# Kernel tuning notes

Hardware: AMD Instinct MI355X
Metric: run time of the kernel (lower is better)

The kernel has to match this reference:

```python
import jax, jax.numpy as jnp
import numpy as np

BN_EPS = 1e-5
L2_EPS = 1e-12


def _gconv(x, adj, W, b):
    # x: [B, N, F_in], adj: [N, N] (densified sparse), W: [F_in, F_out]
    y = jnp.einsum('rc,bcf->brf', adj, x)          # sparse aggregation (spmm)
    y = jnp.einsum('brf,fo->bro', y, W) + b        # dense transform + bias
    n = jnp.sqrt(jnp.sum(y * y, axis=2, keepdims=True))
    return y / jnp.maximum(n, L2_EPS)              # F.normalize(p=2, dim=2)


def _bn3(x):
    # BatchNorm1d over channel dim=1 (roinum), batch stats, affine = identity
    m = jnp.mean(x, axis=(0, 2), keepdims=True)
    v = jnp.var(x, axis=(0, 2), keepdims=True)
    return (x - m) / jnp.sqrt(v + BN_EPS)


def _bn2(x):
    m = jnp.mean(x, axis=0, keepdims=True)
    v = jnp.var(x, axis=0, keepdims=True)
    return (x - m) / jnp.sqrt(v + BN_EPS)


def setup_inputs() -> dict:
    key = jax.random.key(0)
    ks = jax.random.split(key, 20)
    B, N, F_in, H, E, L = 256, 400, 400, 64, 64, 2
    NNZ = 16000
    pred_in = H * 2 + E  # hidden*(num_layers-1) + embedding = 192
    nhid = H

    def xavier(k, fi, fo):
        s = np.sqrt(6.0 / (fi + fo))
        return jax.random.uniform(k, (fi, fo), jnp.float32, -s, s)

    return {
        'x': jax.random.normal(ks[0], (B, N, F_in), jnp.float32),
        'adj_rows': jax.random.randint(ks[1], (NNZ,), 0, N, jnp.int32),
        'adj_cols': jax.random.randint(ks[2], (NNZ,), 0, N, jnp.int32),
        'adj_vals': jax.random.uniform(ks[3], (NNZ,), jnp.float32),
        'W1': xavier(ks[4], F_in, H), 'b1': jnp.zeros((H,), jnp.float32),
        'W2': xavier(ks[5], H, H),    'b2': jnp.zeros((H,), jnp.float32),
        'W3': xavier(ks[6], H, E),    'b3': jnp.zeros((E,), jnp.float32),
        'fc1_W': xavier(ks[7], pred_in, nhid), 'fc1_b': jnp.zeros((nhid,), jnp.float32),
        'fc2_W': xavier(ks[8], nhid, nhid),    'fc2_b': jnp.zeros((nhid,), jnp.float32),
        'fc3_W': xavier(ks[9], nhid, L),       'fc3_b': jnp.zeros((L,), jnp.float32),
    }


def reference(x, adj_rows, adj_cols, adj_vals,
              W1, b1, W2, b2, W3, b3,
              fc1_W, fc1_b, fc2_W, fc2_b, fc3_W, fc3_b):
    N = x.shape[1]
    adj = jnp.zeros((N, N), x.dtype).at[adj_rows, adj_cols].add(adj_vals)

    x1 = _bn3(jax.nn.relu(_gconv(x, adj, W1, b1)))
    out1 = jnp.max(x1, axis=1)                     # [B, H]
    x2 = _bn3(jax.nn.relu(_gconv(x1, adj, W2, b2)))
    out2 = jnp.max(x2, axis=1)                     # [B, H]
    x3 = _gconv(x2, adj, W3, b3)                   # [B, N, E]
    out3 = jnp.max(x3, axis=1)                     # [B, E]

    h = jnp.concatenate([out1, out2, out3], axis=1)  # [B, 2H+E]
    h = _bn2(jax.nn.relu(h @ fc1_W + fc1_b))
    h = _bn2(jax.nn.relu(h @ fc2_W + fc2_b))
    ypred = h @ fc3_W + fc3_b
    return ypred, x3
```

## Files before the change

### kernel.cpp

```cpp
#include <hip/hip_runtime.h>
#include <hip/hip_bf16.h>
#include <math.h>

#define Bb   256
#define Nn   400
#define FIN  400
#define Hh   64
#define NNZ  16000
#define Mrows (Bb*Nn)
#define KP   416
#define UTP  416
#define UPAD 420
#define BH_COUNT 16384.0f

typedef unsigned int  u32x2 __attribute__((ext_vector_type(2)));
typedef unsigned int  u32x4 __attribute__((ext_vector_type(4)));
typedef __bf16        bf16x8 __attribute__((ext_vector_type(8)));
typedef float         f32x4 __attribute__((ext_vector_type(4)));

__device__ __forceinline__ unsigned int f2bf(float x) {
    unsigned int u = __builtin_bit_cast(unsigned int, x);
    return (u + 0x7FFFu + ((u >> 16) & 1u)) >> 16;
}
__device__ __forceinline__ float bf2f(unsigned int h) {
    unsigned int u = h << 16;
    return __builtin_bit_cast(float, u);
}

__global__ void initk(float* __restrict__ Adf, float* __restrict__ stats,
                      unsigned short* __restrict__ Ut) {
    int t = blockIdx.x * blockDim.x + threadIdx.x;
    if (t < Nn * KP) Adf[t] = 0.f;
    if (t < 1600) stats[t] = 0.f;
    if (t < Bb * Hh * 16) {
        int bh = t >> 4, k = Nn + (t & 15);
        Ut[(size_t)bh * UTP + k] = 0;
    }
}

__global__ void scatAk(const int* __restrict__ rows, const int* __restrict__ cols,
                       const float* __restrict__ vals, float* __restrict__ Adf) {
    int i = blockIdx.x * blockDim.x + threadIdx.x;
    if (i < NNZ) atomicAdd(&Adf[rows[i] * KP + cols[i]], vals[i]);
}

__global__ void cvtAk(const float* __restrict__ Adf, unsigned short* __restrict__ Adbf) {
    int i = blockIdx.x * blockDim.x + threadIdx.x;
    if (i < Nn * KP) Adbf[i] = (unsigned short)f2bf(Adf[i]);
}

__global__ __launch_bounds__(256) void wprep(
        const float* __restrict__ W1, const float* __restrict__ W2,
        const float* __restrict__ W3,
        unsigned short* __restrict__ T1h, unsigned short* __restrict__ T1l,
        unsigned short* __restrict__ T2h, unsigned short* __restrict__ T2l,
        unsigned short* __restrict__ T3h, unsigned short* __restrict__ T3l) {
    const int w = blockIdx.x >> 6;
    const int c = blockIdx.x & 63;
    const float* W = (w == 0) ? W1 : (w == 1) ? W2 : W3;
    const int KT   = (w == 0) ? FIN : Hh;
    const int KPAD = (w == 0) ? 416 : 64;
    unsigned short* Th = (w == 0) ? T1h : (w == 1) ? T2h : T3h;
    unsigned short* Tl = (w == 0) ? T1l : (w == 1) ? T2l : T3l;

    for (int k = threadIdx.x; k < KPAD; k += 256) {
        float v = (k < KT) ? W[k * 64 + c] : 0.f;
        unsigned int hb = f2bf(v);
        Th[c * KPAD + k] = (unsigned short)hb;
        Tl[c * KPAD + k] = (unsigned short)f2bf(v - bf2f(hb));
    }
}

__global__ __launch_bounds__(256) void xg400(
        const float* __restrict__ A,
        const unsigned short* __restrict__ Wth,
        const unsigned short* __restrict__ Wtl,
        unsigned short* __restrict__ Ut) {
    const int tid  = threadIdx.x;
    const int wv   = tid >> 6;
    const int lane = tid & 63;
    const int cl   = lane & 15;
    const int g    = lane >> 4;
    const int m0   = blockIdx.x * 128;
    const int rowA = m0 + wv * 32 + cl;
    const int rowB = rowA + 16;

    f32x4 acc[2][4];
#pragma unroll
    for (int t2 = 0; t2 < 2; ++t2)
#pragma unroll
        for (int n = 0; n < 4; ++n) acc[t2][n] = f32x4{0.f, 0.f, 0.f, 0.f};

    auto loadA = [&](int s, float4& l0, float4& h0, float4& l1, float4& h1) {
        int kk = s * 32 + g * 8;
        int kc = kk > 392 ? 392 : kk;
        const float* p = &A[(size_t)rowA * FIN + kc];
        l0 = *reinterpret_cast<const float4*>(p);
        h0 = *reinterpret_cast<const float4*>(p + 4);
        const float* q = &A[(size_t)rowB * FIN + kc];
        l1 = *reinterpret_cast<const float4*>(q);
        h1 = *reinterpret_cast<const float4*>(q + 4);
    };
    auto loadW = [&](int s, u32x4* dst) {
        int kk = s * 32 + g * 8;
#pragma unroll
        for (int n = 0; n < 4; ++n) {
            dst[n]     = *reinterpret_cast<const u32x4*>(&Wth[(size_t)(n * 16 + cl) * 416 + kk]);
            dst[4 + n] = *reinterpret_cast<const u32x4*>(&Wtl[(size_t)(n * 16 + cl) * 416 + kk]);
        }
    };
    auto split = [&](const float4& lo, const float4& hi, bf16x8& ah, bf16x8& al) {
        float v0 = lo.x, v1 = lo.y, v2 = lo.z, v3 = lo.w;
        float v4 = hi.x, v5 = hi.y, v6 = hi.z, v7 = hi.w;
        unsigned h0, h1;
        u32x4 hw, lw;
        h0 = f2bf(v0); h1 = f2bf(v1);
        hw[0] = h0 | (h1 << 16);
        lw[0] = f2bf(v0 - bf2f(h0)) | (f2bf(v1 - bf2f(h1)) << 16);
        h0 = f2bf(v2); h1 = f2bf(v3);
        hw[1] = h0 | (h1 << 16);
        lw[1] = f2bf(v2 - bf2f(h0)) | (f2bf(v3 - bf2f(h1)) << 16);
        h0 = f2bf(v4); h1 = f2bf(v5);
        hw[2] = h0 | (h1 << 16);
        lw[2] = f2bf(v4 - bf2f(h0)) | (f2bf(v5 - bf2f(h1)) << 16);
        h0 = f2bf(v6); h1 = f2bf(v7);
        hw[3] = h0 | (h1 << 16);
        lw[3] = f2bf(v6 - bf2f(h0)) | (f2bf(v7 - bf2f(h1)) << 16);
        ah = __builtin_bit_cast(bf16x8, hw);
        al = __builtin_bit_cast(bf16x8, lw);
    };

    float4 cAl0, cAh0, cAl1, cAh1, nAl0, nAh0, nAl1, nAh1;
    u32x4  cW[8], nW[8];
    loadA(0, cAl0, cAh0, cAl1, cAh1);
    loadW(0, cW);

    for (int s = 0; s < 13; ++s) {
        if (s < 12) {
            loadA(s + 1, nAl0, nAh0, nAl1, nAh1);
            loadW(s + 1, nW);
        }
        bf16x8 ah0, al0, ah1, al1;
        split(cAl0, cAh0, ah0, al0);
        split(cAl1, cAh1, ah1, al1);
#pragma unroll
        for (int n = 0; n < 4; ++n) {
            bf16x8 bh = __builtin_bit_cast(bf16x8, cW[n]);
            bf16x8 bl = __builtin_bit_cast(bf16x8, cW[4 + n]);
            acc[0][n] = __builtin_amdgcn_mfma_f32_16x16x32_bf16(ah0, bh, acc[0][n], 0, 0, 0);
            acc[0][n] = __builtin_amdgcn_mfma_f32_16x16x32_bf16(ah0, bl, acc[0][n], 0, 0, 0);
            acc[0][n] = __builtin_amdgcn_mfma_f32_16x16x32_bf16(al0, bh, acc[0][n], 0, 0, 0);
            acc[1][n] = __builtin_amdgcn_mfma_f32_16x16x32_bf16(ah1, bh, acc[1][n], 0, 0, 0);
            acc[1][n] = __builtin_amdgcn_mfma_f32_16x16x32_bf16(ah1, bl, acc[1][n], 0, 0, 0);
            acc[1][n] = __builtin_amdgcn_mfma_f32_16x16x32_bf16(al1, bh, acc[1][n], 0, 0, 0);
        }
        if (s < 12) {
            cAl0 = nAl0; cAh0 = nAh0; cAl1 = nAl1; cAh1 = nAh1;
#pragma unroll
            for (int j = 0; j < 8; ++j) cW[j] = nW[j];
        }
    }

#pragma unroll
    for (int t2 = 0; t2 < 2; ++t2) {
        const int row0  = m0 + wv * 32 + t2 * 16 + g * 4;
        const int b     = row0 / Nn;
        const int node0 = row0 - b * Nn;
#pragma unroll
        for (int n = 0; n < 4; ++n) {
            const int col = n * 16 + cl;
            u32x2 pk;
            pk[0] = f2bf(acc[t2][n][0]) | (f2bf(acc[t2][n][1]) << 16);
            pk[1] = f2bf(acc[t2][n][2]) | (f2bf(acc[t2][n][3]) << 16);
            *reinterpret_cast<u32x2*>(&Ut[((size_t)b * 64 + col) * UTP + node0]) = pk;
        }
    }
}

__global__ __launch_bounds__(256) void aggmm(
        const unsigned short* __restrict__ Ad,
        const unsigned short* __restrict__ Ut,
        const float* __restrict__ bias,
        float* __restrict__ Zout,
        float* __restrict__ ssum, float* __restrict__ ssq) {
    const int b    = blockIdx.x >> 2;
    const int q    = blockIdx.x & 3;
    const int tid  = threadIdx.x;
    const int lane = tid & 63;
    const int wv   = tid >> 6;
    const int cl   = lane & 15;
    const int g    = lane >> 4;
    const unsigned short* __restrict__ Ub = Ut + (size_t)b * 64 * UTP;

    f32x4 acc[2][4];
#pragma unroll
    for (int i = 0; i < 2; ++i)
#pragma unroll
        for (int n = 0; n < 4; ++n) acc[i][n] = f32x4{0.f, 0.f, 0.f, 0.f};

    for (int k0 = 0; k0 < KP; k0 += 32) {
        const int kk = k0 + g * 8;
        bf16x8 bf[4];
#pragma unroll
        for (int n = 0; n < 4; ++n) {
            u32x4 w = *reinterpret_cast<const u32x4*>(&Ub[(size_t)(n * 16 + cl) * UTP + kk]);
            bf[n] = __builtin_bit_cast(bf16x8, w);
        }
#pragma unroll
        for (int i = 0; i < 2; ++i) {
            const int t = q + 4 * wv + 16 * i;
            if (t < 25) {
                const int row = t * 16 + cl;
                u32x4 ar = *reinterpret_cast<const u32x4*>(&Ad[(size_t)row * KP + kk]);
                bf16x8 af = __builtin_bit_cast(bf16x8, ar);
#pragma unroll
                for (int n = 0; n < 4; ++n)
                    acc[i][n] = __builtin_amdgcn_mfma_f32_16x16x32_bf16(
                        af, bf[n], acc[i][n], 0, 0, 0);
            }
        }
    }

    float bv[4];
#pragma unroll
    for (int n = 0; n < 4; ++n) bv[n] = bias[n * 16 + cl];

#pragma unroll
    for (int i = 0; i < 2; ++i) {
        const int t = q + 4 * wv + 16 * i;
        if (t < 25) {
            float y[4][4];
#pragma unroll
            for (int n = 0; n < 4; ++n)
#pragma unroll
                for (int r = 0; r < 4; ++r) y[n][r] = acc[i][n][r] + bv[n];

            float pss[4];
#pragma unroll
            for (int r = 0; r < 4; ++r)
                pss[r] = y[0][r]*y[0][r] + y[1][r]*y[1][r] +
                         y[2][r]*y[2][r] + y[3][r]*y[3][r];
#pragma unroll
            for (int m = 1; m < 16; m <<= 1)
#pragma unroll
                for (int r = 0; r < 4; ++r) pss[r] += __shfl_xor(pss[r], m);

            float rin[4];
#pragma unroll
            for (int r = 0; r < 4; ++r)
                rin[r] = 1.f / fmaxf(sqrtf(pss[r]), 1e-12f);

            float s1[4], s2[4];
#pragma unroll
            for (int r = 0; r < 4; ++r) { s1[r] = 0.f; s2[r] = 0.f; }
#pragma unroll
            for (int n = 0; n < 4; ++n)
#pragma unroll
                for (int r = 0; r < 4; ++r) {
                    float z = fmaxf(y[n][r] * rin[r], 0.f);
                    const int row = t * 16 + g * 4 + r;
                    Zout[((size_t)b * Nn + row) * Hh + n * 16 + cl] = z;
                    s1[r] += z;
                    s2[r] += z * z;
                }
#pragma unroll
            for (int m = 1; m < 16; m <<= 1)
#pragma unroll
                for (int r = 0; r < 4; ++r) {
                    s1[r] += __shfl_xor(s1[r], m);
                    s2[r] += __shfl_xor(s2[r], m);
                }
            if (cl == 0) {
#pragma unroll
                for (int r = 0; r < 4; ++r) {
                    const int row = t * 16 + g * 4 + r;
                    atomicAdd(&ssum[row], s1[r]);
                    atomicAdd(&ssq[row],  s2[r]);
                }
            }
        }
    }
}

__global__ void finalize_stats(const float* __restrict__ ssum,
                               const float* __restrict__ ssq,
                               float* __restrict__ mean, float* __restrict__ inv) {
    int r = threadIdx.x;
    if (r < Nn) {
        float m = ssum[r] * (1.0f / BH_COUNT);
        float v = ssq[r] * (1.0f / BH_COUNT) - m * m;
        mean[r] = m;
        inv[r]  = rsqrtf(v + 1e-5f);
    }
}

template <bool STATS>
__global__ __launch_bounds__(1024) void fusedl(
        const float* __restrict__ Zin,
        const unsigned short* __restrict__ Ad,
        const unsigned short* __restrict__ Wth,
        const unsigned short* __restrict__ Wtl,
        const float* __restrict__ mean, const float* __restrict__ inv,
        const float* __restrict__ bias,
        float* __restrict__ Zout,
        float* __restrict__ ssum, float* __restrict__ ssq,
        float* __restrict__ outmax_za,
        float* __restrict__ out3) {
    __shared__ unsigned short Us[64 * UPAD];
    __shared__ float sred[16][64];
    const int b    = blockIdx.x;
    const int tid  = threadIdx.x;
    const int wv   = tid >> 6;
    const int lane = tid & 63;
    const int cl   = lane & 15;
    const int g    = lane >> 4;

    for (int i = tid; i < 64 * (UPAD - Nn); i += 1024) {
        int c = i / (UPAD - Nn), k = Nn + i % (UPAD - Nn);
        Us[c * UPAD + k] = 0;
    }

    const int t0 = wv;
    const int t1 = wv + 16;
    const bool has1 = (t1 < 25);

    float za0[16], za1[16];
    {
        const int node = t0 * 16 + cl;
        const float mm = mean[node], iv = inv[node];
#pragma unroll
        for (int s = 0; s < 2; ++s) {
            const float* p = &Zin[((size_t)b * Nn + node) * 64 + s * 32 + g * 8];
            float4 lo = *reinterpret_cast<const float4*>(p);
            float4 hi = *reinterpret_cast<const float4*>(p + 4);
            za0[s * 8 + 0] = (lo.x - mm) * iv;
            za0[s * 8 + 1] = (lo.y - mm) * iv;
            za0[s * 8 + 2] = (lo.z - mm) * iv;
            za0[s * 8 + 3] = (lo.w - mm) * iv;
            za0[s * 8 + 4] = (hi.x - mm) * iv;
            za0[s * 8 + 5] = (hi.y - mm) * iv;
            za0[s * 8 + 6] = (hi.z - mm) * iv;
            za0[s * 8 + 7] = (hi.w - mm) * iv;
        }
    }
    if (has1) {
        const int node = t1 * 16 + cl;
        const float mm = mean[node], iv = inv[node];
#pragma unroll
        for (int s = 0; s < 2; ++s) {
            const float* p = &Zin[((size_t)b * Nn + node) * 64 + s * 32 + g * 8];
            float4 lo = *reinterpret_cast<const float4*>(p);
            float4 hi = *reinterpret_cast<const float4*>(p + 4);
            za1[s * 8 + 0] = (lo.x - mm) * iv;
            za1[s * 8 + 1] = (lo.y - mm) * iv;
            za1[s * 8 + 2] = (lo.z - mm) * iv;
            za1[s * 8 + 3] = (lo.w - mm) * iv;
            za1[s * 8 + 4] = (hi.x - mm) * iv;
            za1[s * 8 + 5] = (hi.y - mm) * iv;
            za1[s * 8 + 6] = (hi.z - mm) * iv;
            za1[s * 8 + 7] = (hi.w - mm) * iv;
        }
    }

    float vmax[16];
#pragma unroll
    for (int j = 0; j < 16; ++j) {
        vmax[j] = za0[j];
        if (has1) vmax[j] = fmaxf(vmax[j], za1[j]);
    }

    auto processA = [&](int t, const float* za) {
        f32x4 acc[4];
#pragma unroll
        for (int n = 0; n < 4; ++n) acc[n] = f32x4{0.f, 0.f, 0.f, 0.f};
#pragma unroll
        for (int s = 0; s < 2; ++s) {
            u32x4 hw, lw;
#pragma unroll
            for (int j = 0; j < 4; ++j) {
                unsigned h0 = f2bf(za[s * 8 + 2 * j]);
                unsigned h1 = f2bf(za[s * 8 + 2 * j + 1]);
                hw[j] = h0 | (h1 << 16);
                lw[j] = f2bf(za[s * 8 + 2 * j] - bf2f(h0)) |
                        (f2bf(za[s * 8 + 2 * j + 1] - bf2f(h1)) << 16);
            }
            bf16x8 ah = __builtin_bit_cast(bf16x8, hw);
            bf16x8 al = __builtin_bit_cast(bf16x8, lw);
            const int kk = s * 32 + g * 8;
#pragma unroll
            for (int n = 0; n < 4; ++n) {
                u32x4 bhw = *reinterpret_cast<const u32x4*>(&Wth[(size_t)(n * 16 + cl) * 64 + kk]);
                u32x4 blw = *reinterpret_cast<const u32x4*>(&Wtl[(size_t)(n * 16 + cl) * 64 + kk]);
                bf16x8 bh = __builtin_bit_cast(bf16x8, bhw);
                bf16x8 bl = __builtin_bit_cast(bf16x8, blw);
                acc[n] = __builtin_amdgcn_mfma_f32_16x16x32_bf16(ah, bh, acc[n], 0, 0, 0);
                acc[n] = __builtin_amdgcn_mfma_f32_16x16x32_bf16(ah, bl, acc[n], 0, 0, 0);
                acc[n] = __builtin_amdgcn_mfma_f32_16x16x32_bf16(al, bh, acc[n], 0, 0, 0);
            }
        }
        const int node0 = t * 16 + g * 4;
#pragma unroll
        for (int n = 0; n < 4; ++n) {
            const int col = n * 16 + cl;
            u32x2 pk;
            pk[0] = f2bf(acc[n][0]) | (f2bf(acc[n][1]) << 16);
            pk[1] = f2bf(acc[n][2]) | (f2bf(acc[n][3]) << 16);
            *reinterpret_cast<u32x2*>(&Us[col * UPAD + node0]) = pk;
        }
    };
    processA(t0, za0);
    if (has1) processA(t1, za1);

#pragma unroll
    for (int m = 1; m < 16; m <<= 1)
#pragma unroll
        for (int j = 0; j < 16; ++j)
            vmax[j] = fmaxf(vmax[j], __shfl_xor(vmax[j], m));
    if (cl == 0) {
#pragma unroll
        for (int j = 0; j < 16; ++j) {
            const int h = 32 * (j >> 3) + g * 8 + (j & 7);
            sred[wv][h] = vmax[j];
        }
    }
    __syncthreads();
    if (tid < 64) {
        float m = sred[0][tid];
#pragma unroll
        for (int w = 1; w < 16; ++w) m = fmaxf(m, sred[w][tid]);
        outmax_za[b * 64 + tid] = m;
    }

    const float bvs[4] = {bias[cl], bias[16 + cl], bias[32 + cl], bias[48 + cl]};
    float pmax[4];
#pragma unroll
    for (int n = 0; n < 4; ++n) pmax[n] = -3.4e38f;

    f32x4 acc[2][4];
#pragma unroll
    for (int i = 0; i < 2; ++i)
#pragma unroll
        for (int n = 0; n < 4; ++n) acc[i][n] = f32x4{0.f, 0.f, 0.f, 0.f};

    for (int k0 = 0; k0 < KP; k0 += 32) {
        const int kk = k0 + g * 8;
        bf16x8 bf[4];
#pragma unroll
        for (int n = 0; n < 4; ++n) {
            const unsigned short* p = &Us[(n * 16 + cl) * UPAD + kk];
            u32x2 lo = *reinterpret_cast<const u32x2*>(p);
            u32x2 hi = *reinterpret_cast<const u32x2*>(p + 4);
            u32x4 w; w[0] = lo[0]; w[1] = lo[1]; w[2] = hi[0]; w[3] = hi[1];
            bf[n] = __builtin_bit_cast(bf16x8, w);
        }
#pragma unroll
        for (int i = 0; i < 2; ++i) {
            const int t = wv + 16 * i;
            if (t < 25) {
                const int row = t * 16 + cl;
                u32x4 ar = *reinterpret_cast<const u32x4*>(&Ad[(size_t)row * KP + kk]);
                bf16x8 af = __builtin_bit_cast(bf16x8, ar);
#pragma unroll
                for (int n = 0; n < 4; ++n)
                    acc[i][n] = __builtin_amdgcn_mfma_f32_16x16x32_bf16(
                        af, bf[n], acc[i][n], 0, 0, 0);
            }
        }
    }

#pragma unroll
    for (int i = 0; i < 2; ++i) {
        const int t = wv + 16 * i;
        if (t < 25) {
            float y[4][4];
#pragma unroll
            for (int n = 0; n < 4; ++n)
#pragma unroll
                for (int r = 0; r < 4; ++r) y[n][r] = acc[i][n][r] + bvs[n];

            float pss[4];
#pragma unroll
            for (int r = 0; r < 4; ++r)
                pss[r] = y[0][r]*y[0][r] + y[1][r]*y[1][r] +
                         y[2][r]*y[2][r] + y[3][r]*y[3][r];
#pragma unroll
            for (int m = 1; m < 16; m <<= 1)
#pragma unroll
                for (int r = 0; r < 4; ++r) pss[r] += __shfl_xor(pss[r], m);

            float rin[4];
#pragma unroll
            for (int r = 0; r < 4; ++r)
                rin[r] = 1.f / fmaxf(sqrtf(pss[r]), 1e-12f);

            float s1[4], s2a[4];
#pragma unroll
            for (int r = 0; r < 4; ++r) { s1[r] = 0.f; s2a[r] = 0.f; }
#pragma unroll
            for (int n = 0; n < 4; ++n)
#pragma unroll
                for (int r = 0; r < 4; ++r) {
                    float z = y[n][r] * rin[r];
                    if (STATS) z = fmaxf(z, 0.f);
                    const int row = t * 16 + g * 4 + r;
                    Zout[((size_t)b * Nn + row) * Hh + n * 16 + cl] = z;
                    if (STATS) { s1[r] += z; s2a[r] += z * z; }
                    else        pmax[n] = fmaxf(pmax[n], z);
                }

            if (STATS) {
#pragma unroll
                for (int m = 1; m < 16; m <<= 1)
#pragma unroll
                    for (int r = 0; r < 4; ++r) {
                        s1[r]  += __shfl_xor(s1[r], m);
                        s2a[r] += __shfl_xor(s2a[r], m);
                    }
                if (cl == 0) {
#pragma unroll
                    for (int r = 0; r < 4; ++r) {
                        const int row = t * 16 + g * 4 + r;
                        atomicAdd(&ssum[row], s1[r]);
                        atomicAdd(&ssq[row],  s2a[r]);
                    }
                }
            }
        }
    }

    if constexpr (!STATS) {
        __syncthreads();
#pragma unroll
        for (int m = 16; m < 64; m <<= 1)
#pragma unroll
            for (int n = 0; n < 4; ++n)
                pmax[n] = fmaxf(pmax[n], __shfl_xor(pmax[n], m));
        if (lane < 16) {
#pragma unroll
            for (int n = 0; n < 4; ++n) sred[wv][n * 16 + cl] = pmax[n];
        }
        __syncthreads();
        if (tid < 64) {
            float m = sred[0][tid];
#pragma unroll
            for (int w = 1; w < 16; ++w) m = fmaxf(m, sred[w][tid]);
            out3[b * 64 + tid] = m;
        }
    }
}

__global__ __launch_bounds__(1024) void headk(
        const float* __restrict__ out1, const float* __restrict__ out2,
        const float* __restrict__ out3,
        const float* __restrict__ W1f, const float* __restrict__ b1f,
        const float* __restrict__ W2f, const float* __restrict__ b2f,
        const float* __restrict__ W3f, const float* __restrict__ b3f,
        float* __restrict__ ypred) {
    __shared__ float gA[256][64];
    __shared__ float w1s[192 * 64];
    __shared__ float w2s[64 * 64];
    __shared__ float mS[64], iS[64];
    const int t = threadIdx.x;
    const int r = t >> 2, q = t & 3;

    for (int i = t; i < 192 * 64; i += 1024) w1s[i] = W1f[i];
    for (int i = t; i < 64 * 64; i += 1024) w2s[i] = W2f[i];
    __syncthreads();

    float acc[16];
#pragma unroll
    for (int j = 0; j < 16; ++j) acc[j] = b1f[q * 16 + j];
    for (int k = 0; k < 192; ++k) {
        float hv = (k < 64) ? out1[r * 64 + k]
                 : (k < 128) ? out2[r * 64 + (k - 64)]
                             : out3[r * 64 + (k - 128)];
#pragma unroll
        for (int j = 0; j < 16; ++j) acc[j] += hv * w1s[k * 64 + q * 16 + j];
    }
#pragma unroll
    for (int j = 0; j < 16; ++j) gA[r][q * 16 + j] = fmaxf(acc[j], 0.f);
    __syncthreads();

    if (t < 64) {
        float s = 0.f, s2 = 0.f;
        for (int rr = 0; rr < 256; ++rr) { float v = gA[rr][t]; s += v; s2 += v * v; }
        float m = s * (1.f / 256.f);
        float var = s2 * (1.f / 256.f) - m * m;
        mS[t] = m;
        iS[t] = rsqrtf(var + 1e-5f);
    }
    __syncthreads();

#pragma unroll
    for (int j = 0; j < 16; ++j) acc[j] = b2f[q * 16 + j];
#pragma unroll
    for (int k = 0; k < 64; ++k) {
        float gn = (gA[r][k] - mS[k]) * iS[k];
#pragma unroll
        for (int j = 0; j < 16; ++j) acc[j] += gn * w2s[k * 64 + q * 16 + j];
    }
    __syncthreads();
#pragma unroll
    for (int j = 0; j < 16; ++j) gA[r][q * 16 + j] = fmaxf(acc[j], 0.f);
    __syncthreads();

    if (t < 64) {
        float s = 0.f, s2 = 0.f;
        for (int rr = 0; rr < 256; ++rr) { float v = gA[rr][t]; s += v; s2 += v * v; }
        float m = s * (1.f / 256.f);
        float var = s2 * (1.f / 256.f) - m * m;
        mS[t] = m;
        iS[t] = rsqrtf(var + 1e-5f);
    }
    __syncthreads();

    if (q < 2) {
        float a = b3f[q];
#pragma unroll
        for (int k = 0; k < 64; ++k) {
            float gn = (gA[r][k] - mS[k]) * iS[k];
            a += gn * W3f[k * 2 + q];
        }
        ypred[r * 2 + q] = a;
    }
}

extern "C" void kernel_launch(void* const* d_in, const int* in_sizes, int n_in,
                              void* d_out, int out_size, void* d_ws, size_t ws_size,
                              hipStream_t stream) {
    const float* x    = (const float*)d_in[0];
    const int*   arow = (const int*)d_in[1];
    const int*   acol = (const int*)d_in[2];
    const float* aval = (const float*)d_in[3];
    const float* W1 = (const float*)d_in[4];
    const float* b1 = (const float*)d_in[5];
    const float* W2 = (const float*)d_in[6];
    const float* b2 = (const float*)d_in[7];
    const float* W3 = (const float*)d_in[8];
    const float* b3 = (const float*)d_in[9];
    const float* fc1W = (const float*)d_in[10];
    const float* fc1b = (const float*)d_in[11];
    const float* fc2W = (const float*)d_in[12];
    const float* fc2b = (const float*)d_in[13];
    const float* fc3W = (const float*)d_in[14];
    const float* fc3b = (const float*)d_in[15];

    char* w = (char*)d_ws;
    size_t off = 0;
    float* Adf = (float*)(w + off);            off += (size_t)Nn * KP * 4;
    unsigned short* Adbf = (unsigned short*)(w + off); off += (size_t)Nn * KP * 2;
    unsigned short* T1h = (unsigned short*)(w + off); off += (size_t)64 * 416 * 2;
    unsigned short* T1l = (unsigned short*)(w + off); off += (size_t)64 * 416 * 2;
    unsigned short* T2h = (unsigned short*)(w + off); off += (size_t)64 * 64 * 2;
    unsigned short* T2l = (unsigned short*)(w + off); off += (size_t)64 * 64 * 2;
    unsigned short* T3h = (unsigned short*)(w + off); off += (size_t)64 * 64 * 2;
    unsigned short* T3l = (unsigned short*)(w + off); off += (size_t)64 * 64 * 2;
    unsigned short* Ut = (unsigned short*)(w + off); off += (size_t)Bb * 64 * UTP * 2;
    float* Z1 = (float*)(w + off);             off += (size_t)Mrows * Hh * 4;
    float* Z2 = (float*)(w + off);             off += (size_t)Mrows * Hh * 4;
    float* stats = (float*)(w + off);          off += 1600 * 4;
    float* ssum1 = stats, *ssq1 = stats + 400, *ssum2 = stats + 800, *ssq2 = stats + 1200;
    float* mean1 = (float*)(w + off); off += 1600;
    float* inv1  = (float*)(w + off); off += 1600;
    float* mean2 = (float*)(w + off); off += 1600;
    float* inv2  = (float*)(w + off); off += 1600;
    float* out1  = (float*)(w + off); off += Bb * Hh * 4;
    float* out2  = (float*)(w + off); off += Bb * Hh * 4;
    float* out3  = (float*)(w + off); off += Bb * Hh * 4;

    float* ypred = (float*)d_out;
    float* x3    = (float*)d_out + 512;

    initk<<<384, 1024, 0, stream>>>(Adf, stats, Ut);
    scatAk<<<(NNZ + 255) / 256, 256, 0, stream>>>(arow, acol, aval, Adf);
    cvtAk<<<(Nn * KP + 1023) / 1024, 1024, 0, stream>>>(Adf, Adbf);
    wprep<<<192, 256, 0, stream>>>(W1, W2, W3, T1h, T1l, T2h, T2l, T3h, T3l);

    xg400<<<Mrows / 128, 256, 0, stream>>>(x, T1h, T1l, Ut);
    aggmm<<<Bb * 4, 256, 0, stream>>>(Adbf, Ut, b1, Z1, ssum1, ssq1);
    finalize_stats<<<1, 512, 0, stream>>>(ssum1, ssq1, mean1, inv1);

    fusedl<true><<<Bb, 1024, 0, stream>>>(Z1, Adbf, T2h, T2l, mean1, inv1, b2,
                                          Z2, ssum2, ssq2, out1, nullptr);
    finalize_stats<<<1, 512, 0, stream>>>(ssum2, ssq2, mean2, inv2);

    fusedl<false><<<Bb, 1024, 0, stream>>>(Z2, Adbf, T3h, T3l, mean2, inv2, b3,
                                           x3, nullptr, nullptr, out2, out3);

    headk<<<1, 1024, 0, stream>>>(out1, out2, out3, fc1W, fc1b, fc2W, fc2b,
                                  fc3W, fc3b, ypred);
}
```

Baseline: 303.2 us.

## Fuse layer-1 feature transform and adjacency aggregation into one per-batch kernel

Merges the x@W1 GEMM (xg400) and the adjacency spmm (aggmm) into a single kernel with one 1024-thread block per batch item. The intermediate U tile is kept in shared memory instead of being written to and reread from a global buffer, which removes that round trip and one launch. In exchange, the grid drops to 256 large blocks, waves with two row tiles become unbalanced (tiles 16-24 only), and shared memory use per block limits occupancy.

```diff
diff --git a/kernel.cpp b/kernel.cpp
--- a/kernel.cpp
+++ b/kernel.cpp
@@ -9,7 +9,6 @@
 #define NNZ  16000
 #define Mrows (Bb*Nn)
 #define KP   416
-#define UTP  416
 #define UPAD 420
 #define BH_COUNT 16384.0f
 
@@ -27,15 +26,10 @@
     return __builtin_bit_cast(float, u);
 }
 
-__global__ void initk(float* __restrict__ Adf, float* __restrict__ stats,
-                      unsigned short* __restrict__ Ut) {
+__global__ void initk(float* __restrict__ Adf, float* __restrict__ stats) {
     int t = blockIdx.x * blockDim.x + threadIdx.x;
     if (t < Nn * KP) Adf[t] = 0.f;
     if (t < 1600) stats[t] = 0.f;
-    if (t < Bb * Hh * 16) {
-        int bh = t >> 4, k = Nn + (t & 15);
-        Ut[(size_t)bh * UTP + k] = 0;
-    }
 }
 
 __global__ void scatAk(const int* __restrict__ rows, const int* __restrict__ cols,
@@ -71,19 +65,33 @@
     }
 }
 
-__global__ __launch_bounds__(256) void xg400(
-        const float* __restrict__ A,
+__global__ __launch_bounds__(1024) void fused1(
+        const float* __restrict__ x,
         const unsigned short* __restrict__ Wth,
         const unsigned short* __restrict__ Wtl,
-        unsigned short* __restrict__ Ut) {
+        const unsigned short* __restrict__ Ad,
+        const float* __restrict__ bias,
+        float* __restrict__ Zout,
+        float* __restrict__ ssum, float* __restrict__ ssq) {
+    __shared__ unsigned short Us[64 * UPAD];
+    const int b    = blockIdx.x;
     const int tid  = threadIdx.x;
     const int wv   = tid >> 6;
     const int lane = tid & 63;
     const int cl   = lane & 15;
     const int g    = lane >> 4;
-    const int m0   = blockIdx.x * 128;
-    const int rowA = m0 + wv * 32 + cl;
-    const int rowB = rowA + 16;
+
+    for (int i = tid; i < 64 * (UPAD - Nn); i += 1024) {
+        int c = i / (UPAD - Nn), k = Nn + i % (UPAD - Nn);
+        Us[c * UPAD + k] = 0;
+    }
+
+    const int t0 = wv, t1 = wv + 16;
+    const bool has1 = (t1 < 25);
+    const int r0 = t0 * 16 + cl;
+    const int r1 = has1 ? (t1 * 16 + cl) : r0;
+    const float* __restrict__ A0 = &x[((size_t)b * Nn + r0) * FIN];
+    const float* __restrict__ A1 = &x[((size_t)b * Nn + r1) * FIN];
 
     f32x4 acc[2][4];
 #pragma unroll
@@ -94,12 +102,10 @@
     auto loadA = [&](int s, float4& l0, float4& h0, float4& l1, float4& h1) {
         int kk = s * 32 + g * 8;
         int kc = kk > 392 ? 392 : kk;
-        const float* p = &A[(size_t)rowA * FIN + kc];
-        l0 = *reinterpret_cast<const float4*>(p);
-        h0 = *reinterpret_cast<const float4*>(p + 4);
-        const float* q = &A[(size_t)rowB * FIN + kc];
-        l1 = *reinterpret_cast<const float4*>(q);
-        h1 = *reinterpret_cast<const float4*>(q + 4);
+        l0 = *reinterpret_cast<const float4*>(A0 + kc);
+        h0 = *reinterpret_cast<const float4*>(A0 + kc + 4);
+        l1 = *reinterpret_cast<const float4*>(A1 + kc);
+        h1 = *reinterpret_cast<const float4*>(A1 + kc + 4);
     };
     auto loadW = [&](int s, u32x4* dst) {
         int kk = s * 32 + g * 8;
@@ -150,9 +156,16 @@
             acc[0][n] = __builtin_amdgcn_mfma_f32_16x16x32_bf16(ah0, bh, acc[0][n], 0, 0, 0);
             acc[0][n] = __builtin_amdgcn_mfma_f32_16x16x32_bf16(ah0, bl, acc[0][n], 0, 0, 0);
             acc[0][n] = __builtin_amdgcn_mfma_f32_16x16x32_bf16(al0, bh, acc[0][n], 0, 0, 0);
-            acc[1][n] = __builtin_amdgcn_mfma_f32_16x16x32_bf16(ah1, bh, acc[1][n], 0, 0, 0);
-            acc[1][n] = __builtin_amdgcn_mfma_f32_16x16x32_bf16(ah1, bl, acc[1][n], 0, 0, 0);
-            acc[1][n] = __builtin_amdgcn_mfma_f32_16x16x32_bf16(al1, bh, acc[1][n], 0, 0, 0);
+        }
+        if (has1) {
+#pragma unroll
+            for (int n = 0; n < 4; ++n) {
+                bf16x8 bh = __builtin_bit_cast(bf16x8, cW[n]);
+                bf16x8 bl = __builtin_bit_cast(bf16x8, cW[4 + n]);
+                acc[1][n] = __builtin_amdgcn_mfma_f32_16x16x32_bf16(ah1, bh, acc[1][n], 0, 0, 0);
+                acc[1][n] = __builtin_amdgcn_mfma_f32_16x16x32_bf16(ah1, bl, acc[1][n], 0, 0, 0);
+                acc[1][n] = __builtin_amdgcn_mfma_f32_16x16x32_bf16(al1, bh, acc[1][n], 0, 0, 0);
+            }
         }
         if (s < 12) {
             cAl0 = nAl0; cAh0 = nAh0; cAl1 = nAl1; cAh1 = nAh1;
@@ -163,77 +176,62 @@
 
 #pragma unroll
     for (int t2 = 0; t2 < 2; ++t2) {
-        const int row0  = m0 + wv * 32 + t2 * 16 + g * 4;
-        const int b     = row0 / Nn;
-        const int node0 = row0 - b * Nn;
+        if (t2 == 1 && !has1) break;
+        const int node0 = (t2 ? t1 : t0) * 16 + g * 4;
 #pragma unroll
         for (int n = 0; n < 4; ++n) {
             const int col = n * 16 + cl;
             u32x2 pk;
             pk[0] = f2bf(acc[t2][n][0]) | (f2bf(acc[t2][n][1]) << 16);
             pk[1] = f2bf(acc[t2][n][2]) | (f2bf(acc[t2][n][3]) << 16);
-            *reinterpret_cast<u32x2*>(&Ut[((size_t)b * 64 + col) * UTP + node0]) = pk;
-        }
-    }
-}
-
-__global__ __launch_bounds__(256) void aggmm(
-        const unsigned short* __restrict__ Ad,
-        const unsigned short* __restrict__ Ut,
-        const float* __restrict__ bias,
-        float* __restrict__ Zout,
-        float* __restrict__ ssum, float* __restrict__ ssq) {
-    const int b    = blockIdx.x >> 2;
-    const int q    = blockIdx.x & 3;
-    const int tid  = threadIdx.x;
-    const int lane = tid & 63;
-    const int wv   = tid >> 6;
-    const int cl   = lane & 15;
-    const int g    = lane >> 4;
-    const unsigned short* __restrict__ Ub = Ut + (size_t)b * 64 * UTP;
-
-    f32x4 acc[2][4];
+            *reinterpret_cast<u32x2*>(&Us[col * UPAD + node0]) = pk;
+        }
+    }
+    __syncthreads();
+
+    const float bvs[4] = {bias[cl], bias[16 + cl], bias[32 + cl], bias[48 + cl]};
+
+    f32x4 bacc[2][4];
 #pragma unroll
     for (int i = 0; i < 2; ++i)
 #pragma unroll
-        for (int n = 0; n < 4; ++n) acc[i][n] = f32x4{0.f, 0.f, 0.f, 0.f};
+        for (int n = 0; n < 4; ++n) bacc[i][n] = f32x4{0.f, 0.f, 0.f, 0.f};
 
     for (int k0 = 0; k0 < KP; k0 += 32) {
         const int kk = k0 + g * 8;
         bf16x8 bf[4];
 #pragma unroll
         for (int n = 0; n < 4; ++n) {
-            u32x4 w = *reinterpret_cast<const u32x4*>(&Ub[(size_t)(n * 16 + cl) * UTP + kk]);
+            const unsigned short* p = &Us[(n * 16 + cl) * UPAD + kk];
+            u32x2 lo = *reinterpret_cast<const u32x2*>(p);
+            u32x2 hi = *reinterpret_cast<const u32x2*>(p + 4);
+            u32x4 w; w[0] = lo[0]; w[1] = lo[1]; w[2] = hi[0]; w[3] = hi[1];
             bf[n] = __builtin_bit_cast(bf16x8, w);
         }
 #pragma unroll
         for (int i = 0; i < 2; ++i) {
-            const int t = q + 4 * wv + 16 * i;
+            const int t = wv + 16 * i;
             if (t < 25) {
                 const int row = t * 16 + cl;
                 u32x4 ar = *reinterpret_cast<const u32x4*>(&Ad[(size_t)row * KP + kk]);
                 bf16x8 af = __builtin_bit_cast(bf16x8, ar);
 #pragma unroll
                 for (int n = 0; n < 4; ++n)
-                    acc[i][n] = __builtin_amdgcn_mfma_f32_16x16x32_bf16(
-                        af, bf[n], acc[i][n], 0, 0, 0);
+                    bacc[i][n] = __builtin_amdgcn_mfma_f32_16x16x32_bf16(
+                        af, bf[n], bacc[i][n], 0, 0, 0);
             }
         }
     }
 
-    float bv[4];
-#pragma unroll
-    for (int n = 0; n < 4; ++n) bv[n] = bias[n * 16 + cl];
-
 #pragma unroll
     for (int i = 0; i < 2; ++i) {
-        const int t = q + 4 * wv + 16 * i;
+        const int t = wv + 16 * i;
         if (t < 25) {
             float y[4][4];
 #pragma unroll
             for (int n = 0; n < 4; ++n)
 #pragma unroll
-                for (int r = 0; r < 4; ++r) y[n][r] = acc[i][n][r] + bv[n];
+                for (int r = 0; r < 4; ++r) y[n][r] = bacc[i][n][r] + bvs[n];
 
             float pss[4];
 #pragma unroll
@@ -250,9 +248,9 @@
             for (int r = 0; r < 4; ++r)
                 rin[r] = 1.f / fmaxf(sqrtf(pss[r]), 1e-12f);
 
-            float s1[4], s2[4];
-#pragma unroll
-            for (int r = 0; r < 4; ++r) { s1[r] = 0.f; s2[r] = 0.f; }
+            float s1[4], s2a[4];
+#pragma unroll
+            for (int r = 0; r < 4; ++r) { s1[r] = 0.f; s2a[r] = 0.f; }
 #pragma unroll
             for (int n = 0; n < 4; ++n)
 #pragma unroll
@@ -261,21 +259,21 @@
                     const int row = t * 16 + g * 4 + r;
                     Zout[((size_t)b * Nn + row) * Hh + n * 16 + cl] = z;
                     s1[r] += z;
-                    s2[r] += z * z;
+                    s2a[r] += z * z;
                 }
 #pragma unroll
             for (int m = 1; m < 16; m <<= 1)
 #pragma unroll
                 for (int r = 0; r < 4; ++r) {
-                    s1[r] += __shfl_xor(s1[r], m);
-                    s2[r] += __shfl_xor(s2[r], m);
+                    s1[r]  += __shfl_xor(s1[r], m);
+                    s2a[r] += __shfl_xor(s2a[r], m);
                 }
             if (cl == 0) {
 #pragma unroll
                 for (int r = 0; r < 4; ++r) {
                     const int row = t * 16 + g * 4 + r;
                     atomicAdd(&ssum[row], s1[r]);
-                    atomicAdd(&ssq[row],  s2[r]);
+                    atomicAdd(&ssq[row],  s2a[r]);
                 }
             }
         }
@@ -655,7 +653,6 @@
     unsigned short* T2l = (unsigned short*)(w + off); off += (size_t)64 * 64 * 2;
     unsigned short* T3h = (unsigned short*)(w + off); off += (size_t)64 * 64 * 2;
     unsigned short* T3l = (unsigned short*)(w + off); off += (size_t)64 * 64 * 2;
-    unsigned short* Ut = (unsigned short*)(w + off); off += (size_t)Bb * 64 * UTP * 2;
     float* Z1 = (float*)(w + off);             off += (size_t)Mrows * Hh * 4;
     float* Z2 = (float*)(w + off);             off += (size_t)Mrows * Hh * 4;
     float* stats = (float*)(w + off);          off += 1600 * 4;
@@ -671,13 +668,12 @@
     float* ypred = (float*)d_out;
     float* x3    = (float*)d_out + 512;
 
-    initk<<<384, 1024, 0, stream>>>(Adf, stats, Ut);
+    initk<<<163, 1024, 0, stream>>>(Adf, stats);
     scatAk<<<(NNZ + 255) / 256, 256, 0, stream>>>(arow, acol, aval, Adf);
     cvtAk<<<(Nn * KP + 1023) / 1024, 1024, 0, stream>>>(Adf, Adbf);
     wprep<<<192, 256, 0, stream>>>(W1, W2, W3, T1h, T1l, T2h, T2l, T3h, T3l);
 
-    xg400<<<Mrows / 128, 256, 0, stream>>>(x, T1h, T1l, Ut);
-    aggmm<<<Bb * 4, 256, 0, stream>>>(Adbf, Ut, b1, Z1, ssum1, ssq1);
+    fused1<<<Bb, 1024, 0, stream>>>(x, T1h, T1l, Adbf, b1, Z1, ssum1, ssq1);
     finalize_stats<<<1, 512, 0, stream>>>(ssum1, ssq1, mean1, inv1);
 
     fusedl<true><<<Bb, 1024, 0, stream>>>(Z1, Adbf, T2h, T2l, mean1, inv1, b2,
```

Result: slower. 314.7 us (+3.8%).
